# Kernel tuning notes

Hardware: AMD Instinct MI355X
Metric: run time of the kernel (lower is better)

The kernel has to match this reference:

```python
import jax, jax.numpy as jnp
import numpy as np

B, N, DIM, H, DH = 2, 2048, 1024, 16, 64

def setup_inputs() -> dict:
    key = jax.random.key(0)
    ks = jax.random.split(key, 7)
    s = 0.02
    return {
        "x": jax.random.normal(ks[0], (B, N, DIM), jnp.float32),
        "pos_emb": jax.random.normal(ks[1], (N, DH), jnp.float32),
        "Wq": jax.random.normal(ks[2], (DIM, H * DH), jnp.float32) * s,
        "Wk": jax.random.normal(ks[3], (DIM, H * DH), jnp.float32) * s,
        "Wv": jax.random.normal(ks[4], (DIM, H * DH), jnp.float32) * s,
        "Wo": jax.random.normal(ks[5], (H * DH, DIM), jnp.float32) * s,
        "bo": jnp.zeros((DIM,), jnp.float32),
    }

def _rotate_half(t):
    t1, t2 = jnp.split(t, 2, axis=-1)
    return jnp.concatenate([-t2, t1], axis=-1)

def _apply_rotary(t, angles):
    # t: [b,h,n,d], angles: [n,d]
    cos = jnp.cos(angles)[None, None]
    sin = jnp.sin(angles)[None, None]
    return t * cos + _rotate_half(t) * sin

def reference(x, pos_emb, Wq, Wk, Wv, Wo, bo):
    b, n, _ = x.shape
    scale = DH ** -0.5
    def split_heads(t):  # [b,n,h*d] -> [b,h,n,d]
        return t.reshape(b, n, H, DH).transpose(0, 2, 1, 3)
    q = split_heads(x @ Wq) * scale
    k = split_heads(x @ Wk)
    v = split_heads(x @ Wv)
    q = _apply_rotary(q, pos_emb)
    k = _apply_rotary(k, pos_emb)
    sim = jnp.einsum('bhid,bhjd->bhij', q, k)
    mask_value = -jnp.finfo(sim.dtype).max
    causal_mask = jnp.triu(jnp.ones((n, n), dtype=bool), 1)
    sim = jnp.where(causal_mask, mask_value, sim)
    attn = jax.nn.softmax(sim, axis=-1)
    out = jnp.einsum('bhij,bhjd->bhid', attn, v)
    out = out.transpose(0, 2, 1, 3).reshape(b, n, H * DH)
    return out @ Wo + bo
```

## Files before the change

### kernel.cpp

```cpp
#include <hip/hip_runtime.h>

#define B_   2
#define N_   2048
#define DIM_ 1024
#define H_   16
#define DH_  64
#define M_   (B_*N_)
#define QKVN (3*DIM_)

typedef __attribute__((ext_vector_type(8)))  short short8;
typedef __attribute__((ext_vector_type(4)))  float floatx4;
typedef __attribute__((ext_vector_type(16))) float floatx16;

__device__ inline unsigned short f2b(float f) {
  union { float f; unsigned u; } v; v.f = f;
  unsigned r = v.u + 0x7fffu + ((v.u >> 16) & 1u);
  return (unsigned short)(r >> 16);
}

__device__ inline unsigned cvtpk(float a, float b) {
  unsigned d;
  asm("v_cvt_pk_bf16_f32 %0, %1, %2" : "=v"(d) : "v"(a), "v"(b));
  return d;
}

__device__ inline floatx4 mfma16(short8 a, short8 b, floatx4 c) {
  return __builtin_amdgcn_mfma_f32_16x16x32_bf16(a, b, c, 0, 0, 0);
}
__device__ inline floatx16 mfma32(short8 a, short8 b, floatx16 c) {
  return __builtin_amdgcn_mfma_f32_32x32x16_bf16(a, b, c, 0, 0, 0);
}

__device__ inline int swz(int row, int byteoff) {
  return row * 64 + (((byteoff) ^ ((row & 7) << 4)) >> 1);
}

__device__ inline void gl_lds16(const void* g, void* l) {
  __builtin_amdgcn_global_load_lds((const __attribute__((address_space(1))) void*)g,
                                   (__attribute__((address_space(3))) void*)l, 16, 0, 0);
}

__device__ inline short8 u4_to_s8(unsigned a, unsigned b, unsigned c, unsigned d) {
  union { unsigned u[4]; short8 s; } v;
  v.u[0] = a; v.u[1] = b; v.u[2] = c; v.u[3] = d;
  return v.s;
}

__global__ void cast_x_kernel(const float* __restrict__ x, unsigned short* __restrict__ xb) {
  int i = blockIdx.x * 256 + threadIdx.x;
  float4 v = ((const float4*)x)[i];
  ushort4 o;
  o.x = f2b(v.x); o.y = f2b(v.y); o.z = f2b(v.z); o.w = f2b(v.w);
  ((ushort4*)xb)[i] = o;
}

__global__ void trig_kernel(const float* __restrict__ pos, float* __restrict__ cs) {
  int i = blockIdx.x * 256 + threadIdx.x;
  float a = pos[i];
  float2 v; v.x = cosf(a); v.y = sinf(a);
  ((float2*)cs)[i] = v;
}

__global__ void transpose_w_kernel(const float* __restrict__ W0, const float* __restrict__ W1,
                                   const float* __restrict__ W2, const float* __restrict__ W3,
                                   unsigned short* __restrict__ T0, unsigned short* __restrict__ T1,
                                   unsigned short* __restrict__ T2, unsigned short* __restrict__ T3) {
  int z = blockIdx.z;
  const float* W = (z == 0) ? W0 : (z == 1) ? W1 : (z == 2) ? W2 : W3;
  unsigned short* T = (z == 0) ? T0 : (z == 1) ? T1 : (z == 2) ? T2 : T3;
  __shared__ float tile[32][33];
  int x = threadIdx.x, y = threadIdx.y;
  int bx = blockIdx.x * 32, by = blockIdx.y * 32;
  #pragma unroll
  for (int i = 0; i < 32; i += 8)
    tile[y + i][x] = W[(size_t)(by + y + i) * 1024 + bx + x];
  __syncthreads();
  #pragma unroll
  for (int i = 0; i < 32; i += 8)
    T[(size_t)(bx + y + i) * 1024 + by + x] = f2b(tile[x][y + i]);
}

template <int MODE>
__global__ __launch_bounds__(256) void gemm_bt_kernel(
    const unsigned short* __restrict__ A, const unsigned short* __restrict__ BT,
    float* __restrict__ C, const float* __restrict__ bias,
    const float* __restrict__ cs,
    unsigned short* __restrict__ qb, unsigned short* __restrict__ kb,
    unsigned short* __restrict__ vtb,
    int M, int N, int K)
{
  __shared__ __align__(16) unsigned short As[128 * 32];
  __shared__ __align__(16) unsigned short Bs[128 * 32];
  int t = threadIdx.x;
  int lane = t & 63, wave = t >> 6;
  int wr = (wave >> 1) * 64, wc = (wave & 1) * 64;

  const unsigned short* Ab = A  + (size_t)(blockIdx.y * 128) * K;
  const unsigned short* Bb = BT + (size_t)(blockIdx.x * 128) * K;

  int sA = wave * 2;
  int grow = (lane >> 2), gcol = (lane & 3) * 8;
  const unsigned short* gA0 = Ab + (size_t)((sA    ) * 16 + grow) * K + gcol;
  const unsigned short* gA1 = Ab + (size_t)((sA + 1) * 16 + grow) * K + gcol;
  const unsigned short* gB0 = Bb + (size_t)((sA    ) * 16 + grow) * K + gcol;
  const unsigned short* gB1 = Bb + (size_t)((sA + 1) * 16 + grow) * K + gcol;
  unsigned short* lA0 = &As[(sA    ) * 512];
  unsigned short* lA1 = &As[(sA + 1) * 512];
  unsigned short* lB0 = &Bs[(sA    ) * 512];
  unsigned short* lB1 = &Bs[(sA + 1) * 512];

  floatx4 acc[4][4];
  #pragma unroll
  for (int i = 0; i < 4; ++i)
    #pragma unroll
    for (int j = 0; j < 4; ++j)
      acc[i][j] = (floatx4){0.f, 0.f, 0.f, 0.f};

  int nk = K >> 5;
  for (int kt = 0; kt < nk; ++kt) {
    if (kt) __syncthreads();
    int ko = kt * 32;
    gl_lds16(gA0 + ko, lA0);
    gl_lds16(gA1 + ko, lA1);
    gl_lds16(gB0 + ko, lB0);
    gl_lds16(gB1 + ko, lB1);
    __syncthreads();
    short8 af[4], bf[4];
    #pragma unroll
    for (int fi = 0; fi < 4; ++fi)
      af[fi] = *(const short8*)&As[(wr + fi * 16 + (lane & 15)) * 32 + (lane >> 4) * 8];
    #pragma unroll
    for (int fj = 0; fj < 4; ++fj)
      bf[fj] = *(const short8*)&Bs[(wc + fj * 16 + (lane & 15)) * 32 + (lane >> 4) * 8];
    __builtin_amdgcn_s_setprio(1);
    #pragma unroll
    for (int fi = 0; fi < 4; ++fi)
      #pragma unroll
      for (int fj = 0; fj < 4; ++fj)
        acc[fi][fj] = mfma16(af[fi], bf[fj], acc[fi][fj]);
    __builtin_amdgcn_s_setprio(0);
  }

  int lane15 = lane & 15;
  int row0 = blockIdx.y * 128 + wr + (lane >> 4) * 4;

  if constexpr (MODE == 0) {
    int col0 = blockIdx.x * 128 + wc + lane15;
    #pragma unroll
    for (int fi = 0; fi < 4; ++fi) {
      #pragma unroll
      for (int fj = 0; fj < 4; ++fj) {
        int col = col0 + fj * 16;
        float bv = bias ? bias[col] : 0.f;
        #pragma unroll
        for (int r = 0; r < 4; ++r) {
          int row = row0 + fi * 16 + r;
          C[(size_t)row * N + col] = acc[fi][fj][r] + bv;
        }
      }
    }
  } else {
    int colbase = blockIdx.x * 128 + wc;
    int region = colbase >> 10;
    int h = (colbase >> 6) & 15;
    if (region < 2) {
      const float qs = (region == 0) ? 0.18033688011112042f : 1.0f;
      unsigned short* dst = (region == 0) ? qb : kb;
      #pragma unroll
      for (int fj = 0; fj < 4; ++fj) {
        int d = fj * 16 + lane15;
        float sgn = (fj < 2) ? -1.f : 1.f;
        #pragma unroll
        for (int fi = 0; fi < 4; ++fi) {
          #pragma unroll
          for (int r = 0; r < 4; ++r) {
            int row = row0 + fi * 16 + r;
            int b = row >> 11, n = row & 2047;
            float2 csv = *(const float2*)&cs[((size_t)n * 64 + d) * 2];
            float a = acc[fi][fj][r], p = acc[fi][fj ^ 2][r];
            dst[(((size_t)(b * 16 + h)) * 2048 + n) * 64 + d] =
                f2b((a * csv.x + sgn * p * csv.y) * qs);
          }
        }
      }
    } else {
      #pragma unroll
      for (int fj = 0; fj < 4; ++fj) {
        int d = fj * 16 + lane15;
        #pragma unroll
        for (int fi = 0; fi < 4; ++fi) {
          int row = row0 + fi * 16;
          int b = row >> 11, n = row & 2047;
          uint2 pk;
          pk.x = cvtpk(acc[fi][fj][0], acc[fi][fj][1]);
          pk.y = cvtpk(acc[fi][fj][2], acc[fi][fj][3]);
          *(uint2*)&vtb[((size_t)(b * 16 + h) * 64 + d) * 2048 + n] = pk;
        }
      }
    }
  }
}

__global__ __launch_bounds__(256) void attn_kernel(
    const unsigned short* __restrict__ qg, const unsigned short* __restrict__ kg,
    const unsigned short* __restrict__ vtg, unsigned short* __restrict__ ctx)
{
  __shared__ __align__(16) unsigned short KV[4][4096];

  int bid = blockIdx.x;
  int bh  = bid & 31;
  int pr  = bid >> 5;
  int t = threadIdx.x, lane = t & 63, wave = t >> 6;
  int lane31 = lane & 31, hi = lane >> 5;
  bool hib = (hi != 0);
  int b = bh >> 4, h = bh & 15;

  const unsigned short* kp = kg  + (size_t)bh * N_ * DH_;
  const unsigned short* vp = vtg + (size_t)bh * 64 * (size_t)N_;

  int srow = t >> 2;
  int scol = (t & 3) * 16;
  int4 kreg0, kreg1, vreg0, vreg1;

#define LOAD_TILE(KV0) do {                                                    \
    kreg0 = *(const int4*)(kp + (size_t)((KV0) + srow) * 64 + scol);           \
    kreg1 = *(const int4*)(kp + (size_t)((KV0) + srow) * 64 + scol + 8);       \
    vreg0 = *(const int4*)(vp + (size_t)srow * N_ + (KV0) + scol);             \
    vreg1 = *(const int4*)(vp + (size_t)srow * N_ + (KV0) + scol + 8);         \
  } while (0)
#define STORE_TILE(BUF) do {                                                   \
    *(int4*)&KV[(BUF)][swz(srow, (t & 3) * 32)]          = kreg0;              \
    *(int4*)&KV[(BUF)][swz(srow, (t & 3) * 32 + 16)]     = kreg1;              \
    *(int4*)&KV[2 + (BUF)][swz(srow, (t & 3) * 32)]      = vreg0;              \
    *(int4*)&KV[2 + (BUF)][swz(srow, (t & 3) * 32 + 16)] = vreg1;              \
  } while (0)

  for (int ci = 0; ci < 2; ++ci) {
    int qc = ci ? pr : (15 - pr);
    int q0 = qc * 128;
    int nt = (qc + 1) * 2;
    int qw0 = q0 + wave * 32;
    int qr  = qw0 + lane31;

    short8 qf[4];
    {
      const unsigned short* qrp = qg + ((size_t)bh * N_ + qr) * DH_;
      #pragma unroll
      for (int ks = 0; ks < 4; ++ks)
        qf[ks] = *(const short8*)(qrp + ks * 16 + hi * 8);
    }

    LOAD_TILE(0);
    STORE_TILE(0);

    floatx16 oa0 = (floatx16)(0.f), oa1 = (floatx16)(0.f);
    float lr = 0.f;

    for (int kt = 0; kt < nt; ++kt) {
      __syncthreads();
      int kv0 = kt * 64;
      bool more = (kt + 1 < nt);
      if (more) LOAD_TILE(kv0 + 64);

      bool active = (kv0 <= qw0 + 31);
      if (active) {
        const unsigned short* Kb = KV[kt & 1];
        const unsigned short* Vb = KV[2 + (kt & 1)];

        floatx16 sa0 = (floatx16)(0.f), sa1 = (floatx16)(0.f);
        __builtin_amdgcn_s_setprio(1);
        #pragma unroll
        for (int ks = 0; ks < 4; ++ks) {
          int bo = ks * 32 + hi * 16;
          short8 kf0 = *(const short8*)&Kb[swz(lane31, bo)];
          short8 kf1 = *(const short8*)&Kb[swz(32 + lane31, bo)];
          sa0 = mfma32(kf0, qf[ks], sa0);
          sa1 = mfma32(kf1, qf[ks], sa1);
        }
        __builtin_amdgcn_s_setprio(0);

        if (kv0 + 63 > qw0) {
          #pragma unroll
          for (int r = 0; r < 16; ++r) {
            int kvA = kv0 + ((r & 3) + 8 * (r >> 2) + 4 * hi);
            if (kvA > qr)      sa0[r] = -3.0e38f;
            if (kvA + 32 > qr) sa1[r] = -3.0e38f;
          }
        }

        float ps = 0.f;
        #pragma unroll
        for (int r = 0; r < 16; ++r) {
          float p0 = exp2f(sa0[r]); sa0[r] = p0; ps += p0;
          float p1 = exp2f(sa1[r]); sa1[r] = p1; ps += p1;
        }
        ps += __shfl_xor(ps, 32);
        lr += ps;

        #pragma unroll
        for (int kvb = 0; kvb < 2; ++kvb) {
          floatx16 sv = (kvb == 0) ? sa0 : sa1;
          unsigned pk0 = cvtpk(sv[0],  sv[1]),  pk1 = cvtpk(sv[2],  sv[3]);
          unsigned pk2 = cvtpk(sv[4],  sv[5]),  pk3 = cvtpk(sv[6],  sv[7]);
          unsigned pk4 = cvtpk(sv[8],  sv[9]),  pk5 = cvtpk(sv[10], sv[11]);
          unsigned pk6 = cvtpk(sv[12], sv[13]), pk7 = cvtpk(sv[14], sv[15]);
          unsigned t0 = hib ? pk0 : pk2, t1 = hib ? pk1 : pk3;
          unsigned t2 = hib ? pk4 : pk6, t3 = hib ? pk5 : pk7;
          unsigned r0 = (unsigned)__shfl_xor((int)t0, 32);
          unsigned r1 = (unsigned)__shfl_xor((int)t1, 32);
          unsigned r2 = (unsigned)__shfl_xor((int)t2, 32);
          unsigned r3 = (unsigned)__shfl_xor((int)t3, 32);
          unsigned o0 = hib ? pk2 : pk0, o1 = hib ? pk3 : pk1;
          unsigned o2 = hib ? pk6 : pk4, o3 = hib ? pk7 : pk5;
          short8 pa = u4_to_s8(hib ? r0 : o0, hib ? r1 : o1, hib ? o0 : r0, hib ? o1 : r1);
          short8 pb = u4_to_s8(hib ? r2 : o2, hib ? r3 : o3, hib ? o2 : r2, hib ? o3 : r3);
          int ksA = kvb * 2, ksB = kvb * 2 + 1;
          short8 v00 = *(const short8*)&Vb[swz(lane31,      ksA * 32 + hi * 16)];
          short8 v01 = *(const short8*)&Vb[swz(32 + lane31, ksA * 32 + hi * 16)];
          short8 v10 = *(const short8*)&Vb[swz(lane31,      ksB * 32 + hi * 16)];
          short8 v11 = *(const short8*)&Vb[swz(32 + lane31, ksB * 32 + hi * 16)];
          __builtin_amdgcn_s_setprio(1);
          oa0 = mfma32(v00, pa, oa0);
          oa1 = mfma32(v01, pa, oa1);
          oa0 = mfma32(v10, pb, oa0);
          oa1 = mfma32(v11, pb, oa1);
          __builtin_amdgcn_s_setprio(0);
        }
      }

      if (more) STORE_TILE((kt + 1) & 1);
    }

    __syncthreads();
    {
      float inv = 1.0f / lr;
      int qrow = wave * 32 + lane31;
      #pragma unroll
      for (int db = 0; db < 2; ++db) {
        floatx16 ov = (db == 0) ? oa0 : oa1;
        #pragma unroll
        for (int a = 0; a < 4; ++a) {
          unsigned w0 = cvtpk(ov[4 * a + 0] * inv, ov[4 * a + 1] * inv);
          unsigned w1 = cvtpk(ov[4 * a + 2] * inv, ov[4 * a + 3] * inv);
          int byteoff = 64 * db + 16 * a + 8 * hi;
          uint2 val; val.x = w0; val.y = w1;
          *(uint2*)&KV[qrow >> 6][(qrow & 63) * 64 + ((byteoff ^ ((qrow & 7) << 4)) >> 1)] = val;
        }
      }
    }
    __syncthreads();
    {
      int r = t >> 1, halfo = (t & 1) * 64;
      const unsigned short* srow_ = &KV[r >> 6][(r & 63) * 64];
      unsigned short* dst = ctx + (size_t)(b * N_ + q0 + r) * DIM_ + h * 64 + (halfo >> 1);
      #pragma unroll
      for (int c = 0; c < 4; ++c) {
        int byteo = halfo + c * 16;
        int4 v = *(const int4*)&srow_[(byteo ^ ((r & 7) << 4)) >> 1];
        *(int4*)(dst + c * 8) = v;
      }
    }
    __syncthreads();
  }
#undef LOAD_TILE
#undef STORE_TILE
}

extern "C" void kernel_launch(void* const* d_in, const int* in_sizes, int n_in,
                              void* d_out, int out_size, void* d_ws, size_t ws_size,
                              hipStream_t stream)
{
  const float* x   = (const float*)d_in[0];
  const float* pos = (const float*)d_in[1];
  const float* Wq  = (const float*)d_in[2];
  const float* Wk  = (const float*)d_in[3];
  const float* Wv  = (const float*)d_in[4];
  const float* Wo  = (const float*)d_in[5];
  const float* bo  = (const float*)d_in[6];
  float* out = (float*)d_out;

  char* w = (char*)d_ws;
  size_t off = 0;
  auto alloc = [&](size_t bytes) {
    char* p = w + off;
    off += (bytes + 255) & ~(size_t)255;
    return p;
  };
  unsigned short* xb  = (unsigned short*)alloc((size_t)M_ * DIM_ * 2);
  unsigned short* WT  = (unsigned short*)alloc((size_t)QKVN * DIM_ * 2);
  unsigned short* WoT = (unsigned short*)alloc((size_t)DIM_ * DIM_ * 2);
  float* cs = (float*)alloc((size_t)N_ * DH_ * 2 * 4);
  unsigned short* qb  = (unsigned short*)alloc((size_t)B_ * H_ * N_ * DH_ * 2);
  unsigned short* kb  = (unsigned short*)alloc((size_t)B_ * H_ * N_ * DH_ * 2);
  unsigned short* vtb = (unsigned short*)alloc((size_t)B_ * H_ * N_ * DH_ * 2);
  unsigned short* ctx = (unsigned short*)alloc((size_t)M_ * DIM_ * 2);

  cast_x_kernel<<<(M_ * DIM_ / 4) / 256, 256, 0, stream>>>(x, xb);
  trig_kernel<<<(N_ * DH_) / 256, 256, 0, stream>>>(pos, cs);
  transpose_w_kernel<<<dim3(32, 32, 4), dim3(32, 8), 0, stream>>>(
      Wq, Wk, Wv, Wo,
      WT, WT + (size_t)DIM_ * DIM_, WT + (size_t)2 * DIM_ * DIM_, WoT);
  gemm_bt_kernel<1><<<dim3(QKVN / 128, M_ / 128), 256, 0, stream>>>(
      xb, WT, nullptr, nullptr, cs, qb, kb, vtb, M_, QKVN, DIM_);
  attn_kernel<<<256, 256, 0, stream>>>(qb, kb, vtb, ctx);
  gemm_bt_kernel<0><<<dim3(DIM_ / 128, M_ / 128), 256, 0, stream>>>(
      ctx, WoT, out, bo, nullptr, nullptr, nullptr, nullptr, M_, DIM_, DIM_);
}
```

Baseline: 231.4 us.

## Stage QKV GEMM epilogue through LDS for coalesced stores; split attention blocks

The QKV GEMM epilogue now writes rotary-applied Q/K and transposed V tiles into shared memory first, then emits 16-byte coalesced row stores to global memory. This replaces scattered 2-byte and 8-byte stores. The attention kernel no longer loops over two paired query chunks per block. It launches 512 blocks, one query chunk each, to raise parallelism, and it drops the paired-chunk load balancing. The added epilogue barriers and LDS traffic are the cost.

```diff
diff --git a/kernel.cpp b/kernel.cpp
--- a/kernel.cpp
+++ b/kernel.cpp
@@ -89,8 +89,9 @@
     unsigned short* __restrict__ vtb,
     int M, int N, int K)
 {
-  __shared__ __align__(16) unsigned short As[128 * 32];
-  __shared__ __align__(16) unsigned short Bs[128 * 32];
+  __shared__ __align__(16) unsigned short SH[2][4096];
+  unsigned short* As = &SH[0][0];
+  unsigned short* Bs = &SH[1][0];
   int t = threadIdx.x;
   int lane = t & 63, wave = t >> 6;
   int wr = (wave >> 1) * 64, wc = (wave & 1) * 64;
@@ -160,42 +161,81 @@
       }
     }
   } else {
+    __syncthreads();
+    unsigned short* ep = &SH[0][0];
     int colbase = blockIdx.x * 128 + wc;
     int region = colbase >> 10;
-    int h = (colbase >> 6) & 15;
+    int bb = (blockIdx.y * 128) >> 11;
     if (region < 2) {
       const float qs = (region == 0) ? 0.18033688011112042f : 1.0f;
-      unsigned short* dst = (region == 0) ? qb : kb;
-      #pragma unroll
-      for (int fj = 0; fj < 4; ++fj) {
-        int d = fj * 16 + lane15;
-        float sgn = (fj < 2) ? -1.f : 1.f;
+      unsigned short* dstb = (region == 0) ? qb : kb;
+      int h = (colbase >> 6) & 15;
+      #pragma unroll
+      for (int h2 = 0; h2 < 2; ++h2) {
         #pragma unroll
-        for (int fi = 0; fi < 4; ++fi) {
+        for (int fi2 = 0; fi2 < 2; ++fi2) {
+          int fi = h2 * 2 + fi2;
           #pragma unroll
-          for (int r = 0; r < 4; ++r) {
-            int row = row0 + fi * 16 + r;
-            int b = row >> 11, n = row & 2047;
-            float2 csv = *(const float2*)&cs[((size_t)n * 64 + d) * 2];
-            float a = acc[fi][fj][r], p = acc[fi][fj ^ 2][r];
-            dst[(((size_t)(b * 16 + h)) * 2048 + n) * 64 + d] =
-                f2b((a * csv.x + sgn * p * csv.y) * qs);
+          for (int fj = 0; fj < 4; ++fj) {
+            int d = fj * 16 + lane15;
+            float sgn = (fj < 2) ? -1.f : 1.f;
+            #pragma unroll
+            for (int r = 0; r < 4; ++r) {
+              int n = (row0 + fi * 16 + r) & 2047;
+              float2 csv = *(const float2*)&cs[((size_t)n * 64 + d) * 2];
+              float a = acc[fi][fj][r], p = acc[fi][fj ^ 2][r];
+              int nloc = fi2 * 16 + ((lane >> 4) & 3) * 4 + r;
+              ep[wave * 2048 + nloc * 64 + d] = f2b((a * csv.x + sgn * p * csv.y) * qs);
+            }
           }
         }
+        __syncthreads();
+        {
+          int r2 = lane >> 1, half = lane & 1;
+          int n_glob = blockIdx.y * 128 + wr + h2 * 32 + r2;
+          int nn = n_glob & 2047;
+          unsigned short* dst = dstb + (((size_t)(bb * 16 + h)) * 2048 + nn) * 64 + half * 32;
+          const unsigned short* srcp = ep + wave * 2048 + r2 * 64 + half * 32;
+          #pragma unroll
+          for (int c = 0; c < 4; ++c)
+            *(int4*)(dst + c * 8) = *(const int4*)(srcp + c * 8);
+        }
+        __syncthreads();
       }
     } else {
-      #pragma unroll
-      for (int fj = 0; fj < 4; ++fj) {
-        int d = fj * 16 + lane15;
-        #pragma unroll
-        for (int fi = 0; fi < 4; ++fi) {
-          int row = row0 + fi * 16;
-          int b = row >> 11, n = row & 2047;
-          uint2 pk;
-          pk.x = cvtpk(acc[fi][fj][0], acc[fi][fj][1]);
-          pk.y = cvtpk(acc[fi][fj][2], acc[fi][fj][3]);
-          *(uint2*)&vtb[((size_t)(b * 16 + h) * 64 + d) * 2048 + n] = pk;
-        }
+      int n0 = (blockIdx.y * 128) & 2047;
+      int hA = ((blockIdx.x * 128) >> 6) & 15;
+      #pragma unroll
+      for (int nh = 0; nh < 2; ++nh) {
+        if ((wave >> 1) == nh) {
+          #pragma unroll
+          for (int fi = 0; fi < 4; ++fi) {
+            #pragma unroll
+            for (int fj = 0; fj < 4; ++fj) {
+              int d = fj * 16 + lane15;
+              int sw = (d & 7) << 3;
+              #pragma unroll
+              for (int r = 0; r < 4; ++r) {
+                int nl = fi * 16 + ((lane >> 4) & 3) * 4 + r;
+                ep[(wave & 1) * 4096 + d * 64 + (nl ^ sw)] = f2b(acc[fi][fj][r]);
+              }
+            }
+          }
+        }
+        __syncthreads();
+        {
+          int hh = t >> 7, d = (t >> 1) & 63, half = t & 1;
+          int sw = (d & 7) << 3;
+          const unsigned short* srcp = ep + hh * 4096 + d * 64;
+          unsigned short* dst = vtb + (((size_t)(bb * 16 + hA + hh)) * 64 + d) * 2048
+                                    + n0 + nh * 64 + half * 32;
+          #pragma unroll
+          for (int c = 0; c < 4; ++c) {
+            int off = (half * 32 + c * 8) ^ sw;
+            *(int4*)(dst + c * 8) = *(const int4*)(srcp + off);
+          }
+        }
+        __syncthreads();
       }
     }
   }
@@ -209,7 +249,7 @@
 
   int bid = blockIdx.x;
   int bh  = bid & 31;
-  int pr  = bid >> 5;
+  int qc  = (bid < 256) ? (15 - (bid >> 5)) : ((bid - 256) >> 5);
   int t = threadIdx.x, lane = t & 63, wave = t >> 6;
   int lane31 = lane & 31, hi = lane >> 5;
   bool hib = (hi != 0);
@@ -235,132 +275,128 @@
     *(int4*)&KV[2 + (BUF)][swz(srow, (t & 3) * 32 + 16)] = vreg1;              \
   } while (0)
 
-  for (int ci = 0; ci < 2; ++ci) {
-    int qc = ci ? pr : (15 - pr);
-    int q0 = qc * 128;
-    int nt = (qc + 1) * 2;
-    int qw0 = q0 + wave * 32;
-    int qr  = qw0 + lane31;
-
-    short8 qf[4];
-    {
-      const unsigned short* qrp = qg + ((size_t)bh * N_ + qr) * DH_;
-      #pragma unroll
-      for (int ks = 0; ks < 4; ++ks)
-        qf[ks] = *(const short8*)(qrp + ks * 16 + hi * 8);
-    }
-
-    LOAD_TILE(0);
-    STORE_TILE(0);
-
-    floatx16 oa0 = (floatx16)(0.f), oa1 = (floatx16)(0.f);
-    float lr = 0.f;
-
-    for (int kt = 0; kt < nt; ++kt) {
-      __syncthreads();
-      int kv0 = kt * 64;
-      bool more = (kt + 1 < nt);
-      if (more) LOAD_TILE(kv0 + 64);
-
-      bool active = (kv0 <= qw0 + 31);
-      if (active) {
-        const unsigned short* Kb = KV[kt & 1];
-        const unsigned short* Vb = KV[2 + (kt & 1)];
-
-        floatx16 sa0 = (floatx16)(0.f), sa1 = (floatx16)(0.f);
-        __builtin_amdgcn_s_setprio(1);
-        #pragma unroll
-        for (int ks = 0; ks < 4; ++ks) {
-          int bo = ks * 32 + hi * 16;
-          short8 kf0 = *(const short8*)&Kb[swz(lane31, bo)];
-          short8 kf1 = *(const short8*)&Kb[swz(32 + lane31, bo)];
-          sa0 = mfma32(kf0, qf[ks], sa0);
-          sa1 = mfma32(kf1, qf[ks], sa1);
-        }
-        __builtin_amdgcn_s_setprio(0);
-
-        if (kv0 + 63 > qw0) {
-          #pragma unroll
-          for (int r = 0; r < 16; ++r) {
-            int kvA = kv0 + ((r & 3) + 8 * (r >> 2) + 4 * hi);
-            if (kvA > qr)      sa0[r] = -3.0e38f;
-            if (kvA + 32 > qr) sa1[r] = -3.0e38f;
-          }
-        }
-
-        float ps = 0.f;
+  int q0 = qc * 128;
+  int nt = (qc + 1) * 2;
+  int qw0 = q0 + wave * 32;
+  int qr  = qw0 + lane31;
+
+  short8 qf[4];
+  {
+    const unsigned short* qrp = qg + ((size_t)bh * N_ + qr) * DH_;
+    #pragma unroll
+    for (int ks = 0; ks < 4; ++ks)
+      qf[ks] = *(const short8*)(qrp + ks * 16 + hi * 8);
+  }
+
+  LOAD_TILE(0);
+  STORE_TILE(0);
+
+  floatx16 oa0 = (floatx16)(0.f), oa1 = (floatx16)(0.f);
+  float lr = 0.f;
+
+  for (int kt = 0; kt < nt; ++kt) {
+    __syncthreads();
+    int kv0 = kt * 64;
+    bool more = (kt + 1 < nt);
+    if (more) LOAD_TILE(kv0 + 64);
+
+    bool active = (kv0 <= qw0 + 31);
+    if (active) {
+      const unsigned short* Kb = KV[kt & 1];
+      const unsigned short* Vb = KV[2 + (kt & 1)];
+
+      floatx16 sa0 = (floatx16)(0.f), sa1 = (floatx16)(0.f);
+      __builtin_amdgcn_s_setprio(1);
+      #pragma unroll
+      for (int ks = 0; ks < 4; ++ks) {
+        int bo = ks * 32 + hi * 16;
+        short8 kf0 = *(const short8*)&Kb[swz(lane31, bo)];
+        short8 kf1 = *(const short8*)&Kb[swz(32 + lane31, bo)];
+        sa0 = mfma32(kf0, qf[ks], sa0);
+        sa1 = mfma32(kf1, qf[ks], sa1);
+      }
+      __builtin_amdgcn_s_setprio(0);
+
+      if (kv0 + 63 > qw0) {
         #pragma unroll
         for (int r = 0; r < 16; ++r) {
-          float p0 = exp2f(sa0[r]); sa0[r] = p0; ps += p0;
-          float p1 = exp2f(sa1[r]); sa1[r] = p1; ps += p1;
-        }
-        ps += __shfl_xor(ps, 32);
-        lr += ps;
-
-        #pragma unroll
-        for (int kvb = 0; kvb < 2; ++kvb) {
-          floatx16 sv = (kvb == 0) ? sa0 : sa1;
-          unsigned pk0 = cvtpk(sv[0],  sv[1]),  pk1 = cvtpk(sv[2],  sv[3]);
-          unsigned pk2 = cvtpk(sv[4],  sv[5]),  pk3 = cvtpk(sv[6],  sv[7]);
-          unsigned pk4 = cvtpk(sv[8],  sv[9]),  pk5 = cvtpk(sv[10], sv[11]);
-          unsigned pk6 = cvtpk(sv[12], sv[13]), pk7 = cvtpk(sv[14], sv[15]);
-          unsigned t0 = hib ? pk0 : pk2, t1 = hib ? pk1 : pk3;
-          unsigned t2 = hib ? pk4 : pk6, t3 = hib ? pk5 : pk7;
-          unsigned r0 = (unsigned)__shfl_xor((int)t0, 32);
-          unsigned r1 = (unsigned)__shfl_xor((int)t1, 32);
-          unsigned r2 = (unsigned)__shfl_xor((int)t2, 32);
-          unsigned r3 = (unsigned)__shfl_xor((int)t3, 32);
-          unsigned o0 = hib ? pk2 : pk0, o1 = hib ? pk3 : pk1;
-          unsigned o2 = hib ? pk6 : pk4, o3 = hib ? pk7 : pk5;
-          short8 pa = u4_to_s8(hib ? r0 : o0, hib ? r1 : o1, hib ? o0 : r0, hib ? o1 : r1);
-          short8 pb = u4_to_s8(hib ? r2 : o2, hib ? r3 : o3, hib ? o2 : r2, hib ? o3 : r3);
-          int ksA = kvb * 2, ksB = kvb * 2 + 1;
-          short8 v00 = *(const short8*)&Vb[swz(lane31,      ksA * 32 + hi * 16)];
-          short8 v01 = *(const short8*)&Vb[swz(32 + lane31, ksA * 32 + hi * 16)];
-          short8 v10 = *(const short8*)&Vb[swz(lane31,      ksB * 32 + hi * 16)];
-          short8 v11 = *(const short8*)&Vb[swz(32 + lane31, ksB * 32 + hi * 16)];
-          __builtin_amdgcn_s_setprio(1);
-          oa0 = mfma32(v00, pa, oa0);
-          oa1 = mfma32(v01, pa, oa1);
-          oa0 = mfma32(v10, pb, oa0);
-          oa1 = mfma32(v11, pb, oa1);
-          __builtin_amdgcn_s_setprio(0);
-        }
-      }
-
-      if (more) STORE_TILE((kt + 1) & 1);
+          int kvA = kv0 + ((r & 3) + 8 * (r >> 2) + 4 * hi);
+          if (kvA > qr)      sa0[r] = -3.0e38f;
+          if (kvA + 32 > qr) sa1[r] = -3.0e38f;
+        }
+      }
+
+      float ps = 0.f;
+      #pragma unroll
+      for (int r = 0; r < 16; ++r) {
+        float p0 = exp2f(sa0[r]); sa0[r] = p0; ps += p0;
+        float p1 = exp2f(sa1[r]); sa1[r] = p1; ps += p1;
+      }
+      ps += __shfl_xor(ps, 32);
+      lr += ps;
+
+      #pragma unroll
+      for (int kvb = 0; kvb < 2; ++kvb) {
+        floatx16 sv = (kvb == 0) ? sa0 : sa1;
+        unsigned pk0 = cvtpk(sv[0],  sv[1]),  pk1 = cvtpk(sv[2],  sv[3]);
+        unsigned pk2 = cvtpk(sv[4],  sv[5]),  pk3 = cvtpk(sv[6],  sv[7]);
+        unsigned pk4 = cvtpk(sv[8],  sv[9]),  pk5 = cvtpk(sv[10], sv[11]);
+        unsigned pk6 = cvtpk(sv[12], sv[13]), pk7 = cvtpk(sv[14], sv[15]);
+        unsigned t0 = hib ? pk0 : pk2, t1 = hib ? pk1 : pk3;
+        unsigned t2 = hib ? pk4 : pk6, t3 = hib ? pk5 : pk7;
+        unsigned r0 = (unsigned)__shfl_xor((int)t0, 32);
+        unsigned r1 = (unsigned)__shfl_xor((int)t1, 32);
+        unsigned r2 = (unsigned)__shfl_xor((int)t2, 32);
+        unsigned r3 = (unsigned)__shfl_xor((int)t3, 32);
+        unsigned o0 = hib ? pk2 : pk0, o1 = hib ? pk3 : pk1;
+        unsigned o2 = hib ? pk6 : pk4, o3 = hib ? pk7 : pk5;
+        short8 pa = u4_to_s8(hib ? r0 : o0, hib ? r1 : o1, hib ? o0 : r0, hib ? o1 : r1);
+        short8 pb = u4_to_s8(hib ? r2 : o2, hib ? r3 : o3, hib ? o2 : r2, hib ? o3 : r3);
+        int ksA = kvb * 2, ksB = kvb * 2 + 1;
+        short8 v00 = *(const short8*)&Vb[swz(lane31,      ksA * 32 + hi * 16)];
+        short8 v01 = *(const short8*)&Vb[swz(32 + lane31, ksA * 32 + hi * 16)];
+        short8 v10 = *(const short8*)&Vb[swz(lane31,      ksB * 32 + hi * 16)];
+        short8 v11 = *(const short8*)&Vb[swz(32 + lane31, ksB * 32 + hi * 16)];
+        __builtin_amdgcn_s_setprio(1);
+        oa0 = mfma32(v00, pa, oa0);
+        oa1 = mfma32(v01, pa, oa1);
+        oa0 = mfma32(v10, pb, oa0);
+        oa1 = mfma32(v11, pb, oa1);
+        __builtin_amdgcn_s_setprio(0);
+      }
     }
 
-    __syncthreads();
-    {
-      float inv = 1.0f / lr;
-      int qrow = wave * 32 + lane31;
-      #pragma unroll
-      for (int db = 0; db < 2; ++db) {
-        floatx16 ov = (db == 0) ? oa0 : oa1;
-        #pragma unroll
-        for (int a = 0; a < 4; ++a) {
-          unsigned w0 = cvtpk(ov[4 * a + 0] * inv, ov[4 * a + 1] * inv);
-          unsigned w1 = cvtpk(ov[4 * a + 2] * inv, ov[4 * a + 3] * inv);
-          int byteoff = 64 * db + 16 * a + 8 * hi;
-          uint2 val; val.x = w0; val.y = w1;
-          *(uint2*)&KV[qrow >> 6][(qrow & 63) * 64 + ((byteoff ^ ((qrow & 7) << 4)) >> 1)] = val;
-        }
+    if (more) STORE_TILE((kt + 1) & 1);
+  }
+
+  __syncthreads();
+  {
+    float inv = 1.0f / lr;
+    int qrow = wave * 32 + lane31;
+    #pragma unroll
+    for (int db = 0; db < 2; ++db) {
+      floatx16 ov = (db == 0) ? oa0 : oa1;
+      #pragma unroll
+      for (int a = 0; a < 4; ++a) {
+        unsigned w0 = cvtpk(ov[4 * a + 0] * inv, ov[4 * a + 1] * inv);
+        unsigned w1 = cvtpk(ov[4 * a + 2] * inv, ov[4 * a + 3] * inv);
+        int byteoff = 64 * db + 16 * a + 8 * hi;
+        uint2 val; val.x = w0; val.y = w1;
+        *(uint2*)&KV[qrow >> 6][(qrow & 63) * 64 + ((byteoff ^ ((qrow & 7) << 4)) >> 1)] = val;
       }
     }
-    __syncthreads();
-    {
-      int r = t >> 1, halfo = (t & 1) * 64;
-      const unsigned short* srow_ = &KV[r >> 6][(r & 63) * 64];
-      unsigned short* dst = ctx + (size_t)(b * N_ + q0 + r) * DIM_ + h * 64 + (halfo >> 1);
-      #pragma unroll
-      for (int c = 0; c < 4; ++c) {
-        int byteo = halfo + c * 16;
-        int4 v = *(const int4*)&srow_[(byteo ^ ((r & 7) << 4)) >> 1];
-        *(int4*)(dst + c * 8) = v;
-      }
+  }
+  __syncthreads();
+  {
+    int r = t >> 1, halfo = (t & 1) * 64;
+    const unsigned short* srow_ = &KV[r >> 6][(r & 63) * 64];
+    unsigned short* dst = ctx + (size_t)(b * N_ + q0 + r) * DIM_ + h * 64 + (halfo >> 1);
+    #pragma unroll
+    for (int c = 0; c < 4; ++c) {
+      int byteo = halfo + c * 16;
+      int4 v = *(const int4*)&srow_[(byteo ^ ((r & 7) << 4)) >> 1];
+      *(int4*)(dst + c * 8) = v;
     }
-    __syncthreads();
   }
 #undef LOAD_TILE
 #undef STORE_TILE
@@ -402,7 +438,7 @@
       WT, WT + (size_t)DIM_ * DIM_, WT + (size_t)2 * DIM_ * DIM_, WoT);
   gemm_bt_kernel<1><<<dim3(QKVN / 128, M_ / 128), 256, 0, stream>>>(
       xb, WT, nullptr, nullptr, cs, qb, kb, vtb, M_, QKVN, DIM_);
-  attn_kernel<<<256, 256, 0, stream>>>(qb, kb, vtb, ctx);
+  attn_kernel<<<512, 256, 0, stream>>>(qb, kb, vtb, ctx);
   gemm_bt_kernel<0><<<dim3(DIM_ / 128, M_ / 128), 256, 0, stream>>>(
       ctx, WoT, out, bo, nullptr, nullptr, nullptr, nullptr, M_, DIM_, DIM_);
 }
```

Result: no change. 227.9 us (-1.5%).
